# Kernel tuning notes

Measured on AMD Instinct MI355X. Metric: run time of the kernel, lower is better.

The kernel has to match this reference:

```python
import jax, jax.numpy as jnp
import numpy as np

B, S, MAX_K, MID, V = 4, 512, 32, 32, 32000


def _lin(x, W, b):
    # torch nn.Linear convention: W is [out, in]
    return x @ W.T + b


def _label_count_segment(vals):
    """Distinct-label counts over prefixes [0:1],[0:2],...,[0:K] of the kNN labels."""
    Bv, Sv, K = vals.shape
    mask = jnp.triu(jnp.ones((K, K), dtype=bool), k=1)  # [K,K], True above diagonal
    # row i of expand keeps labels [0:i+1], rest filled with -1 (as in masked_fill)
    ev = jnp.where(mask, jnp.array(-1, vals.dtype), vals[:, :, None, :])  # [B,S,K,K]
    s = jnp.sort(ev, axis=-1)
    # zero-out adjacent duplicates (keep first occurrence)
    dedup = jnp.concatenate([s[..., :1], s[..., 1:] * (s[..., 1:] != s[..., :-1])], axis=-1)
    cnt = (dedup != 0).sum(-1)  # [B,S,K]
    cnt = cnt.at[..., :-1].add(-1)  # remove the single surviving -1 for rows 0..K-2
    return cnt


def setup_inputs():
    key = jax.random.key(0)
    ks = jax.random.split(key, 16)
    tgt_index = jax.random.randint(ks[0], (B, S, MAX_K), 0, V)
    knn_dists = jax.random.uniform(ks[1], (B, S, MAX_K), jnp.float32, 1e-3, 10.0)
    knn_key_feature = jax.random.uniform(ks[2], (B, S, MAX_K), jnp.float32, 1e-4, 1.0)
    network_probs = jax.random.uniform(ks[3], (B, S, V), jnp.float32, 1e-6, 1.0)
    network_probs = network_probs / network_probs.sum(-1, keepdims=True)
    network_select_probs = jax.random.uniform(ks[4], (B, S, MAX_K), jnp.float32, 1e-6, 1e-2)
    init = lambda k, shape: 0.02 * jax.random.normal(k, shape, jnp.float32)
    return {
        "tgt_index": tgt_index,
        "knn_dists": knn_dists,
        "knn_key_feature": knn_key_feature,
        "network_probs": network_probs,
        "network_select_probs": network_select_probs,
        # distance_func: Linear(2K+8, 1)
        "W_func": init(ks[5], (1, 2 * MAX_K + 8)), "b_func": init(ks[6], (1,)),
        # distance_fc1: Linear(2,4) -> Tanh -> Linear(4,1)
        "W1a": init(ks[7], (4, 2)), "b1a": init(ks[8], (4,)),
        "W1b": init(ks[9], (1, 4)), "b1b": init(ks[10], (1,)),
        # distance_fc2: Linear(2K, mid) -> Tanh -> Linear(mid, 2)
        "W2a": init(ks[11], (MID, 2 * MAX_K)), "b2a": init(ks[12], (MID,)),
        "W2b": init(ks[13], (2, MID)), "b2b": init(ks[14], (2,)),
    }


def reference(tgt_index, knn_dists, knn_key_feature, network_probs, network_select_probs,
              W_func, b_func, W1a, b1a, W1b, b1b, W2a, b2a, W2b, b2b):
    Bv, Sv, K = knn_dists.shape
    Vv = network_probs.shape[-1]
    label_counts = _label_count_segment(tgt_index)  # [B,S,K] int
    log_key = jnp.log(knn_key_feature)
    log_sel = jnp.log(network_select_probs)
    all_key_feature = jnp.stack([log_key, log_sel], axis=-1)  # [B,S,K,2]
    top_prob, _ = jax.lax.top_k(network_probs, 8)  # [B,S,8]
    knn_feat = jnp.concatenate([knn_dists, label_counts.astype(knn_dists.dtype)], -1)  # [B,S,2K]
    noise_logit = _lin(jnp.tanh(_lin(all_key_feature, W1a, b1a)), W1b, b1b).squeeze(-1)  # [B,S,K]
    sim_in = jnp.concatenate([jnp.log(top_prob), log_key, log_sel], -1)  # [B,S,2K+8]
    sim_lambda = _lin(sim_in, W_func, b_func)  # [B,S,1]
    lambda_logit = _lin(jnp.tanh(_lin(knn_feat, W2a, b2a)), W2b, b2b)  # [B,S,2]
    knn_lambda = jax.nn.softmax(jnp.concatenate([lambda_logit[..., :1], sim_lambda], -1), -1)[..., :1]
    tempe = jax.nn.sigmoid(lambda_logit[..., 1:2])  # [B,S,1]
    probs = jax.nn.softmax(-knn_dists * tempe + noise_logit, -1)  # [B,S,K]
    bi = jnp.arange(Bv)[:, None, None]
    si = jnp.arange(Sv)[None, :, None]
    knn_prob = jnp.zeros((Bv, Sv, Vv), probs.dtype).at[bi, si, tgt_index].set(probs)
    return knn_prob, knn_lambda
```

## Files before the change

kernel.cpp:

```cpp
#include <hip/hip_runtime.h>

typedef unsigned long long ull;
typedef float f4 __attribute__((ext_vector_type(4)));

#define TOKENS 2048
#define KNN    32
#define VOCAB  32000
#define CAP    2048

#define INSK(key) do {                                                       \
    ull k_ = (key);                                                          \
    if (k_ > c7) {                                                           \
        ull tmp_;                                                            \
        if (k_ > c0) { tmp_ = c0; c0 = k_; k_ = tmp_; }                      \
        if (k_ > c1) { tmp_ = c1; c1 = k_; k_ = tmp_; }                      \
        if (k_ > c2) { tmp_ = c2; c2 = k_; k_ = tmp_; }                      \
        if (k_ > c3) { tmp_ = c3; c3 = k_; k_ = tmp_; }                      \
        if (k_ > c4) { tmp_ = c4; c4 = k_; k_ = tmp_; }                      \
        if (k_ > c5) { tmp_ = c5; c5 = k_; k_ = tmp_; }                      \
        if (k_ > c6) { tmp_ = c6; c6 = k_; k_ = tmp_; }                      \
        c7 = (k_ > c7) ? k_ : c7;                                            \
    }                                                                        \
} while (0)

#define INSF(vv) do {                                                        \
    float x_ = (vv);                                                         \
    if (x_ > t7) {                                                           \
        float h_;                                                            \
        h_ = fmaxf(t0, x_); x_ = fminf(t0, x_); t0 = h_;                     \
        h_ = fmaxf(t1, x_); x_ = fminf(t1, x_); t1 = h_;                     \
        h_ = fmaxf(t2, x_); x_ = fminf(t2, x_); t2 = h_;                     \
        h_ = fmaxf(t3, x_); x_ = fminf(t3, x_); t3 = h_;                     \
        h_ = fmaxf(t4, x_); x_ = fminf(t4, x_); t4 = h_;                     \
        h_ = fmaxf(t5, x_); x_ = fminf(t5, x_); t5 = h_;                     \
        h_ = fmaxf(t6, x_); x_ = fminf(t6, x_); t6 = h_;                     \
        t7 = fmaxf(t7, x_);                                                  \
    }                                                                        \
} while (0)

#define MAX4(v_) fmaxf(fmaxf(v_.x, v_.y), fmaxf(v_.z, v_.w))

#define COLLECT(v_) do {                                                     \
    if (v_.x >= T) { int p = atomicAdd(&s_n, 1); if (p < CAP) s_cand[p] = v_.x; } \
    if (v_.y >= T) { int p = atomicAdd(&s_n, 1); if (p < CAP) s_cand[p] = v_.y; } \
    if (v_.z >= T) { int p = atomicAdd(&s_n, 1); if (p < CAP) s_cand[p] = v_.z; } \
    if (v_.w >= T) { int p = atomicAdd(&s_n, 1); if (p < CAP) s_cand[p] = v_.w; } \
} while (0)

#define BATCH8(kb) do {                                                      \
    f4 v0 = __builtin_nontemporal_load(np4 + tid + (((kb)+0) << 8));         \
    f4 v1 = __builtin_nontemporal_load(np4 + tid + (((kb)+1) << 8));         \
    f4 v2 = __builtin_nontemporal_load(np4 + tid + (((kb)+2) << 8));         \
    f4 v3 = __builtin_nontemporal_load(np4 + tid + (((kb)+3) << 8));         \
    f4 v4 = __builtin_nontemporal_load(np4 + tid + (((kb)+4) << 8));         \
    f4 v5 = __builtin_nontemporal_load(np4 + tid + (((kb)+5) << 8));         \
    f4 v6 = __builtin_nontemporal_load(np4 + tid + (((kb)+6) << 8));         \
    f4 v7 = __builtin_nontemporal_load(np4 + tid + (((kb)+7) << 8));         \
    __builtin_nontemporal_store(z4, o4 + tid + (((kb)+0) << 8));             \
    __builtin_nontemporal_store(z4, o4 + tid + (((kb)+1) << 8));             \
    __builtin_nontemporal_store(z4, o4 + tid + (((kb)+2) << 8));             \
    __builtin_nontemporal_store(z4, o4 + tid + (((kb)+3) << 8));             \
    __builtin_nontemporal_store(z4, o4 + tid + (((kb)+4) << 8));             \
    __builtin_nontemporal_store(z4, o4 + tid + (((kb)+5) << 8));             \
    __builtin_nontemporal_store(z4, o4 + tid + (((kb)+6) << 8));             \
    __builtin_nontemporal_store(z4, o4 + tid + (((kb)+7) << 8));             \
    float m01 = fmaxf(MAX4(v0), MAX4(v1));                                   \
    float m23 = fmaxf(MAX4(v2), MAX4(v3));                                   \
    float m45 = fmaxf(MAX4(v4), MAX4(v5));                                   \
    float m67 = fmaxf(MAX4(v6), MAX4(v7));                                   \
    m = fmaxf(m, fmaxf(fmaxf(m01, m23), fmaxf(m45, m67)));                   \
} while (0)

__global__ __launch_bounds__(256, 6)
void rc_kernel(const int*   __restrict__ tgt_index,
               const float* __restrict__ knn_dists,
               const float* __restrict__ knn_key,
               const float* __restrict__ net_probs,
               const float* __restrict__ net_sel,
               const float* __restrict__ W_func, const float* __restrict__ b_func,
               const float* __restrict__ W1a,    const float* __restrict__ b1a,
               const float* __restrict__ W1b,    const float* __restrict__ b1b,
               const float* __restrict__ W2a,    const float* __restrict__ b2a,
               const float* __restrict__ W2b,    const float* __restrict__ b2b,
               float* __restrict__ out)
{
    const int t   = blockIdx.x;
    const int tid = threadIdx.x;

    __shared__ float s_max[256];
    __shared__ float s_cand[CAP];
    __shared__ int   s_n;
    __shared__ float s_thr;
    __shared__ float s_top8[8];

    if (tid == 0) s_n = 0;

    int   tg = 0;
    float d = 0.f, lk = 0.f, ls = 0.f;
    if (tid < KNN) {
        tg = tgt_index[t * KNN + tid];
        d  = knn_dists[t * KNN + tid];
        lk = logf(knn_key[t * KNN + tid]);
        ls = logf(net_sel[t * KNN + tid]);
        s_tgt_store: ;
    }
    __shared__ int   s_tgt[KNN];
    __shared__ float s_dist[KNN];
    __shared__ float s_cnt[KNN];
    if (tid < KNN) { s_tgt[tid] = tg; s_dist[tid] = d; }

    const f4* np4 = (const f4*)(net_probs + (size_t)t * VOCAB);
    f4*       o4  = (f4*)(out + (size_t)t * VOCAB);
    const f4  z4  = (f4){0.f, 0.f, 0.f, 0.f};
    float m = 0.f;

    BATCH8(0);
    BATCH8(8);
    BATCH8(16);
    {
        f4 v0 = __builtin_nontemporal_load(np4 + tid + (24 << 8));
        f4 v1 = __builtin_nontemporal_load(np4 + tid + (25 << 8));
        f4 v2 = __builtin_nontemporal_load(np4 + tid + (26 << 8));
        f4 v3 = __builtin_nontemporal_load(np4 + tid + (27 << 8));
        f4 v4 = __builtin_nontemporal_load(np4 + tid + (28 << 8));
        f4 v5 = __builtin_nontemporal_load(np4 + tid + (29 << 8));
        f4 v6 = __builtin_nontemporal_load(np4 + tid + (30 << 8));
        __builtin_nontemporal_store(z4, o4 + tid + (24 << 8));
        __builtin_nontemporal_store(z4, o4 + tid + (25 << 8));
        __builtin_nontemporal_store(z4, o4 + tid + (26 << 8));
        __builtin_nontemporal_store(z4, o4 + tid + (27 << 8));
        __builtin_nontemporal_store(z4, o4 + tid + (28 << 8));
        __builtin_nontemporal_store(z4, o4 + tid + (29 << 8));
        __builtin_nontemporal_store(z4, o4 + tid + (30 << 8));
        float m01 = fmaxf(MAX4(v0), MAX4(v1));
        float m23 = fmaxf(MAX4(v2), MAX4(v3));
        float m45 = fmaxf(MAX4(v4), MAX4(v5));
        m = fmaxf(m, fmaxf(fmaxf(m01, m23), fmaxf(m45, MAX4(v6))));
    }
    if (tid < 64) {
        f4 v = __builtin_nontemporal_load(np4 + tid + (31 << 8));
        __builtin_nontemporal_store(z4, o4 + tid + (31 << 8));
        m = fmaxf(m, MAX4(v));
    }
    s_max[tid] = m;
    __syncthreads();

    if (tid < 64) {
        ull c0 = 0, c1 = 0, c2 = 0, c3 = 0, c4 = 0, c5 = 0, c6 = 0, c7 = 0;
        #pragma unroll
        for (int k = 0; k < 4; ++k) {
            int idx = tid + (k << 6);
            ull key = (((ull)__float_as_uint(s_max[idx])) << 32) | (unsigned)idx;
            INSK(key);
        }
        ull g = 0;
        for (int r = 0; r < 8; ++r) {
            g = c0;
            #pragma unroll
            for (int off = 1; off < 64; off <<= 1) {
                ull o = __shfl_xor(g, off);
                if (o > g) g = o;
            }
            if (c0 == g) {
                c0 = c1; c1 = c2; c2 = c3; c3 = c4; c4 = c5; c5 = c6; c6 = c7; c7 = 0;
            }
        }
        if (tid == 0) s_thr = __uint_as_float((unsigned)(g >> 32));
    }
    __syncthreads();
    const float T = s_thr;

    if (m >= T) {
        for (int k = 0; k < 31; ++k) {
            f4 v = np4[tid + (k << 8)];
            COLLECT(v);
        }
        if (tid < 64) {
            f4 v = np4[tid + (31 << 8)];
            COLLECT(v);
        }
    }
    __syncthreads();
    const int n = s_n;

    if (n <= CAP) {
        if (tid < 64) {
            ull c0 = 0, c1 = 0, c2 = 0, c3 = 0, c4 = 0, c5 = 0, c6 = 0, c7 = 0;
            for (int i = tid; i < n; i += 64) {
                ull key = (((ull)__float_as_uint(s_cand[i])) << 32) | (unsigned)i;
                INSK(key);
            }
            for (int r = 0; r < 8; ++r) {
                ull g = c0;
                #pragma unroll
                for (int off = 1; off < 64; off <<= 1) {
                    ull o = __shfl_xor(g, off);
                    if (o > g) g = o;
                }
                if (c0 == g && g != 0ULL) {
                    c0 = c1; c1 = c2; c2 = c3; c3 = c4; c4 = c5; c5 = c6; c6 = c7; c7 = 0;
                }
                if (tid == 0) s_top8[r] = __uint_as_float((unsigned)(g >> 32));
            }
        }
    } else {
        float t0 = 0.f, t1 = 0.f, t2 = 0.f, t3 = 0.f,
              t4 = 0.f, t5 = 0.f, t6 = 0.f, t7 = 0.f;
        for (int k = 0; k < 31; ++k) {
            f4 v = np4[tid + (k << 8)];
            if (MAX4(v) > t7) { INSF(v.x); INSF(v.y); INSF(v.z); INSF(v.w); }
        }
        if (tid < 64) {
            f4 v = np4[tid + (31 << 8)];
            if (MAX4(v) > t7) { INSF(v.x); INSF(v.y); INSF(v.z); INSF(v.w); }
        }
        __syncthreads();
        s_cand[tid * 8 + 0] = t0;  s_cand[tid * 8 + 1] = t1;
        s_cand[tid * 8 + 2] = t2;  s_cand[tid * 8 + 3] = t3;
        s_cand[tid * 8 + 4] = t4;  s_cand[tid * 8 + 5] = t5;
        s_cand[tid * 8 + 6] = t6;  s_cand[tid * 8 + 7] = t7;
        __syncthreads();
        if (tid < 64) {
            ull c0 = 0, c1 = 0, c2 = 0, c3 = 0, c4 = 0, c5 = 0, c6 = 0, c7 = 0;
            for (int k = 0; k < 32; ++k) {
                int idx = tid + (k << 6);
                ull key = (((ull)__float_as_uint(s_cand[idx])) << 32) | (unsigned)idx;
                INSK(key);
            }
            for (int r = 0; r < 8; ++r) {
                ull g = c0;
                #pragma unroll
                for (int off = 1; off < 64; off <<= 1) {
                    ull o = __shfl_xor(g, off);
                    if (o > g) g = o;
                }
                if (c0 == g) {
                    c0 = c1; c1 = c2; c2 = c3; c3 = c4; c4 = c5; c5 = c6; c6 = c7; c7 = 0;
                }
                if (tid == 0) s_top8[r] = __uint_as_float((unsigned)(g >> 32));
            }
        }
    }
    __syncthreads();

    if (tid < KNN) {
        int fo = (tg != 0) ? 1 : 0;
        if (fo) {
            for (int j = 0; j < tid; ++j)
                if (s_tgt[j] == tg) { fo = 0; break; }
        }
        int c = fo;
        #pragma unroll
        for (int off = 1; off < KNN; off <<= 1) {
            int n2 = __shfl_up(c, off, KNN);
            if (tid >= off) c += n2;
        }
        s_cnt[tid] = (float)c;
    }
    __syncthreads();

    if (tid < KNN) {
        float noise = b1b[0];
        #pragma unroll
        for (int j = 0; j < 4; ++j) {
            float z = tanhf(W1a[2 * j] * lk + W1a[2 * j + 1] * ls + b1a[j]);
            noise += W1b[j] * z;
        }

        float sp = W_func[8 + tid] * lk + W_func[40 + tid] * ls;
        if (tid < 8) sp += W_func[tid] * logf(s_top8[tid]);
        #pragma unroll
        for (int off = 16; off; off >>= 1) sp += __shfl_xor(sp, off, KNN);
        float sim = sp + b_func[0];

        float h = b2a[tid];
        const float* wr = W2a + tid * 64;
        #pragma unroll 8
        for (int i = 0; i < KNN; ++i) h += wr[i] * s_dist[i];
        #pragma unroll 8
        for (int i = 0; i < KNN; ++i) h += wr[KNN + i] * s_cnt[i];
        h = tanhf(h);
        float p0 = W2b[tid] * h;
        float p1 = W2b[KNN + tid] * h;
        #pragma unroll
        for (int off = 16; off; off >>= 1) {
            p0 += __shfl_xor(p0, off, KNN);
            p1 += __shfl_xor(p1, off, KNN);
        }
        float l0 = p0 + b2b[0];
        float l1 = p1 + b2b[1];

        float tempe = 1.f / (1.f + expf(-l1));
        float lam   = 1.f / (1.f + expf(-(l0 - sim)));

        float logit = -d * tempe + noise;
        float mx = logit;
        #pragma unroll
        for (int off = 16; off; off >>= 1) mx = fmaxf(mx, __shfl_xor(mx, off, KNN));
        float e = expf(logit - mx);
        float se = e;
        #pragma unroll
        for (int off = 16; off; off >>= 1) se += __shfl_xor(se, off, KNN);
        float p = e / se;

        bool wrte = true;
        for (int j = tid + 1; j < KNN; ++j)
            if (s_tgt[j] == tg) { wrte = false; break; }
        if (wrte) out[(size_t)t * VOCAB + tg] = p;

        if (tid == 0) out[(size_t)TOKENS * VOCAB + t] = lam;
    }
}

extern "C" void kernel_launch(void* const* d_in, const int* in_sizes, int n_in,
                              void* d_out, int out_size, void* d_ws, size_t ws_size,
                              hipStream_t stream) {
    rc_kernel<<<TOKENS, 256, 0, stream>>>(
        (const int*)  d_in[0],
        (const float*)d_in[1],
        (const float*)d_in[2],
        (const float*)d_in[3],
        (const float*)d_in[4],
        (const float*)d_in[5],  (const float*)d_in[6],
        (const float*)d_in[7],  (const float*)d_in[8],
        (const float*)d_in[9],  (const float*)d_in[10],
        (const float*)d_in[11], (const float*)d_in[12],
        (const float*)d_in[13], (const float*)d_in[14],
        (float*)d_out);
}
```

Baseline: 134.6 us.

## Split fused kernel into scan, zero-fill and final kernels via workspace

```diff
diff --git a/kernel.cpp b/kernel.cpp
--- a/kernel.cpp
+++ b/kernel.cpp
@@ -6,7 +6,7 @@
 #define TOKENS 2048
 #define KNN    32
 #define VOCAB  32000
-#define CAP    2048
+#define CAP    512
 
 #define INSK(key) do {                                                       \
     ull k_ = (key);                                                          \
@@ -48,22 +48,14 @@
 } while (0)
 
 #define BATCH8(kb) do {                                                      \
-    f4 v0 = __builtin_nontemporal_load(np4 + tid + (((kb)+0) << 8));         \
-    f4 v1 = __builtin_nontemporal_load(np4 + tid + (((kb)+1) << 8));         \
-    f4 v2 = __builtin_nontemporal_load(np4 + tid + (((kb)+2) << 8));         \
-    f4 v3 = __builtin_nontemporal_load(np4 + tid + (((kb)+3) << 8));         \
-    f4 v4 = __builtin_nontemporal_load(np4 + tid + (((kb)+4) << 8));         \
-    f4 v5 = __builtin_nontemporal_load(np4 + tid + (((kb)+5) << 8));         \
-    f4 v6 = __builtin_nontemporal_load(np4 + tid + (((kb)+6) << 8));         \
-    f4 v7 = __builtin_nontemporal_load(np4 + tid + (((kb)+7) << 8));         \
-    __builtin_nontemporal_store(z4, o4 + tid + (((kb)+0) << 8));             \
-    __builtin_nontemporal_store(z4, o4 + tid + (((kb)+1) << 8));             \
-    __builtin_nontemporal_store(z4, o4 + tid + (((kb)+2) << 8));             \
-    __builtin_nontemporal_store(z4, o4 + tid + (((kb)+3) << 8));             \
-    __builtin_nontemporal_store(z4, o4 + tid + (((kb)+4) << 8));             \
-    __builtin_nontemporal_store(z4, o4 + tid + (((kb)+5) << 8));             \
-    __builtin_nontemporal_store(z4, o4 + tid + (((kb)+6) << 8));             \
-    __builtin_nontemporal_store(z4, o4 + tid + (((kb)+7) << 8));             \
+    f4 v0 = np4[tid + (((kb)+0) << 8)];                                      \
+    f4 v1 = np4[tid + (((kb)+1) << 8)];                                      \
+    f4 v2 = np4[tid + (((kb)+2) << 8)];                                      \
+    f4 v3 = np4[tid + (((kb)+3) << 8)];                                      \
+    f4 v4 = np4[tid + (((kb)+4) << 8)];                                      \
+    f4 v5 = np4[tid + (((kb)+5) << 8)];                                      \
+    f4 v6 = np4[tid + (((kb)+6) << 8)];                                      \
+    f4 v7 = np4[tid + (((kb)+7) << 8)];                                      \
     float m01 = fmaxf(MAX4(v0), MAX4(v1));                                   \
     float m23 = fmaxf(MAX4(v2), MAX4(v3));                                   \
     float m45 = fmaxf(MAX4(v4), MAX4(v5));                                   \
@@ -71,18 +63,8 @@
     m = fmaxf(m, fmaxf(fmaxf(m01, m23), fmaxf(m45, m67)));                   \
 } while (0)
 
-__global__ __launch_bounds__(256, 6)
-void rc_kernel(const int*   __restrict__ tgt_index,
-               const float* __restrict__ knn_dists,
-               const float* __restrict__ knn_key,
-               const float* __restrict__ net_probs,
-               const float* __restrict__ net_sel,
-               const float* __restrict__ W_func, const float* __restrict__ b_func,
-               const float* __restrict__ W1a,    const float* __restrict__ b1a,
-               const float* __restrict__ W1b,    const float* __restrict__ b1b,
-               const float* __restrict__ W2a,    const float* __restrict__ b2a,
-               const float* __restrict__ W2b,    const float* __restrict__ b2b,
-               float* __restrict__ out)
+__global__ __launch_bounds__(256, 8)
+void k_scan(const float* __restrict__ net_probs, float* __restrict__ ws)
 {
     const int t   = blockIdx.x;
     const int tid = threadIdx.x;
@@ -95,51 +77,27 @@
 
     if (tid == 0) s_n = 0;
 
-    int   tg = 0;
-    float d = 0.f, lk = 0.f, ls = 0.f;
-    if (tid < KNN) {
-        tg = tgt_index[t * KNN + tid];
-        d  = knn_dists[t * KNN + tid];
-        lk = logf(knn_key[t * KNN + tid]);
-        ls = logf(net_sel[t * KNN + tid]);
-        s_tgt_store: ;
-    }
-    __shared__ int   s_tgt[KNN];
-    __shared__ float s_dist[KNN];
-    __shared__ float s_cnt[KNN];
-    if (tid < KNN) { s_tgt[tid] = tg; s_dist[tid] = d; }
-
     const f4* np4 = (const f4*)(net_probs + (size_t)t * VOCAB);
-    f4*       o4  = (f4*)(out + (size_t)t * VOCAB);
-    const f4  z4  = (f4){0.f, 0.f, 0.f, 0.f};
+
     float m = 0.f;
-
     BATCH8(0);
     BATCH8(8);
     BATCH8(16);
     {
-        f4 v0 = __builtin_nontemporal_load(np4 + tid + (24 << 8));
-        f4 v1 = __builtin_nontemporal_load(np4 + tid + (25 << 8));
-        f4 v2 = __builtin_nontemporal_load(np4 + tid + (26 << 8));
-        f4 v3 = __builtin_nontemporal_load(np4 + tid + (27 << 8));
-        f4 v4 = __builtin_nontemporal_load(np4 + tid + (28 << 8));
-        f4 v5 = __builtin_nontemporal_load(np4 + tid + (29 << 8));
-        f4 v6 = __builtin_nontemporal_load(np4 + tid + (30 << 8));
-        __builtin_nontemporal_store(z4, o4 + tid + (24 << 8));
-        __builtin_nontemporal_store(z4, o4 + tid + (25 << 8));
-        __builtin_nontemporal_store(z4, o4 + tid + (26 << 8));
-        __builtin_nontemporal_store(z4, o4 + tid + (27 << 8));
-        __builtin_nontemporal_store(z4, o4 + tid + (28 << 8));
-        __builtin_nontemporal_store(z4, o4 + tid + (29 << 8));
-        __builtin_nontemporal_store(z4, o4 + tid + (30 << 8));
+        f4 v0 = np4[tid + (24 << 8)];
+        f4 v1 = np4[tid + (25 << 8)];
+        f4 v2 = np4[tid + (26 << 8)];
+        f4 v3 = np4[tid + (27 << 8)];
+        f4 v4 = np4[tid + (28 << 8)];
+        f4 v5 = np4[tid + (29 << 8)];
+        f4 v6 = np4[tid + (30 << 8)];
         float m01 = fmaxf(MAX4(v0), MAX4(v1));
         float m23 = fmaxf(MAX4(v2), MAX4(v3));
         float m45 = fmaxf(MAX4(v4), MAX4(v5));
         m = fmaxf(m, fmaxf(fmaxf(m01, m23), fmaxf(m45, MAX4(v6))));
     }
     if (tid < 64) {
-        f4 v = __builtin_nontemporal_load(np4 + tid + (31 << 8));
-        __builtin_nontemporal_store(z4, o4 + tid + (31 << 8));
+        f4 v = np4[tid + (31 << 8)];
         m = fmaxf(m, MAX4(v));
     }
     s_max[tid] = m;
@@ -214,33 +172,83 @@
             f4 v = np4[tid + (31 << 8)];
             if (MAX4(v) > t7) { INSF(v.x); INSF(v.y); INSF(v.z); INSF(v.w); }
         }
-        __syncthreads();
-        s_cand[tid * 8 + 0] = t0;  s_cand[tid * 8 + 1] = t1;
-        s_cand[tid * 8 + 2] = t2;  s_cand[tid * 8 + 3] = t3;
-        s_cand[tid * 8 + 4] = t4;  s_cand[tid * 8 + 5] = t5;
-        s_cand[tid * 8 + 6] = t6;  s_cand[tid * 8 + 7] = t7;
-        __syncthreads();
-        if (tid < 64) {
-            ull c0 = 0, c1 = 0, c2 = 0, c3 = 0, c4 = 0, c5 = 0, c6 = 0, c7 = 0;
-            for (int k = 0; k < 32; ++k) {
-                int idx = tid + (k << 6);
-                ull key = (((ull)__float_as_uint(s_cand[idx])) << 32) | (unsigned)idx;
-                INSK(key);
-            }
-            for (int r = 0; r < 8; ++r) {
-                ull g = c0;
+        for (int r = 0; r < 8; ++r) {
+            s_max[tid] = t0;
+            __syncthreads();
+            if (tid < 64) {
+                float g = s_max[tid];
+                g = fmaxf(g, s_max[tid + 64]);
+                g = fmaxf(g, s_max[tid + 128]);
+                g = fmaxf(g, s_max[tid + 192]);
                 #pragma unroll
-                for (int off = 1; off < 64; off <<= 1) {
-                    ull o = __shfl_xor(g, off);
-                    if (o > g) g = o;
-                }
-                if (c0 == g) {
-                    c0 = c1; c1 = c2; c2 = c3; c3 = c4; c4 = c5; c5 = c6; c6 = c7; c7 = 0;
-                }
-                if (tid == 0) s_top8[r] = __uint_as_float((unsigned)(g >> 32));
-            }
-        }
-    }
+                for (int off = 1; off < 64; off <<= 1)
+                    g = fmaxf(g, __shfl_xor(g, off));
+                if (tid == 0) { s_thr = g; s_top8[r] = g; }
+            }
+            __syncthreads();
+            float g = s_thr;
+            ull mask = __ballot(t0 == g);
+            __shared__ int s_win;
+            if (tid == 0) s_win = 0x7fffffff;
+            __syncthreads();
+            if (t0 == g) atomicMin(&s_win, tid);
+            __syncthreads();
+            if (tid == s_win) {
+                t0 = t1; t1 = t2; t2 = t3; t3 = t4; t4 = t5; t5 = t6; t6 = t7; t7 = 0.f;
+            }
+            __syncthreads();
+            (void)mask;
+        }
+    }
+    __syncthreads();
+
+    if (tid < 8) ws[(size_t)t * 8 + tid] = s_top8[tid];
+}
+
+__global__ __launch_bounds__(256, 8)
+void k_zero(float* __restrict__ out)
+{
+    const int t   = blockIdx.x;
+    const int tid = threadIdx.x;
+    f4*      o4 = (f4*)(out + (size_t)t * VOCAB);
+    const f4 z4 = (f4){0.f, 0.f, 0.f, 0.f};
+    #pragma unroll
+    for (int k = 0; k < 31; ++k) o4[tid + (k << 8)] = z4;
+    if (tid < 64) o4[tid + (31 << 8)] = z4;
+}
+
+__global__ __launch_bounds__(256, 8)
+void k2_final(const int*   __restrict__ tgt_index,
+              const float* __restrict__ knn_dists,
+              const float* __restrict__ knn_key,
+              const float* __restrict__ net_sel,
+              const float* __restrict__ W_func, const float* __restrict__ b_func,
+              const float* __restrict__ W1a,    const float* __restrict__ b1a,
+              const float* __restrict__ W1b,    const float* __restrict__ b1b,
+              const float* __restrict__ W2a,    const float* __restrict__ b2a,
+              const float* __restrict__ W2b,    const float* __restrict__ b2b,
+              const float* __restrict__ ws,
+              float* __restrict__ out)
+{
+    const int t   = blockIdx.x;
+    const int tid = threadIdx.x;
+
+    __shared__ int   s_tgt[KNN];
+    __shared__ float s_dist[KNN];
+    __shared__ float s_cnt[KNN];
+    __shared__ float s_top8[8];
+
+    int   tg = 0;
+    float d = 0.f, lk = 0.f, ls = 0.f;
+    if (tid < KNN) {
+        tg = tgt_index[t * KNN + tid];
+        d  = knn_dists[t * KNN + tid];
+        lk = logf(knn_key[t * KNN + tid]);
+        ls = logf(net_sel[t * KNN + tid]);
+        s_tgt[tid]  = tg;
+        s_dist[tid] = d;
+    }
+    if (tid < 8) s_top8[tid] = ws[(size_t)t * 8 + tid];
     __syncthreads();
 
     if (tid < KNN) {
@@ -315,16 +323,20 @@
 extern "C" void kernel_launch(void* const* d_in, const int* in_sizes, int n_in,
                               void* d_out, int out_size, void* d_ws, size_t ws_size,
                               hipStream_t stream) {
-    rc_kernel<<<TOKENS, 256, 0, stream>>>(
+    float* ws = (float*)d_ws;
+
+    k_scan<<<TOKENS, 256, 0, stream>>>((const float*)d_in[3], ws);
+    k_zero<<<TOKENS, 256, 0, stream>>>((float*)d_out);
+    k2_final<<<TOKENS, 256, 0, stream>>>(
         (const int*)  d_in[0],
         (const float*)d_in[1],
         (const float*)d_in[2],
-        (const float*)d_in[3],
         (const float*)d_in[4],
         (const float*)d_in[5],  (const float*)d_in[6],
         (const float*)d_in[7],  (const float*)d_in[8],
         (const float*)d_in[9],  (const float*)d_in[10],
         (const float*)d_in[11], (const float*)d_in[12],
         (const float*)d_in[13], (const float*)d_in[14],
+        ws,
         (float*)d_out);
 }
```

After: 147.1 us. 9.3% more time.
